# Kernel tuning notes

Hardware: AMD Instinct MI355X
Metric: run time of the kernel (lower is better)

## Reference

```python
import jax, jax.numpy as jnp
import numpy as np
import math

EMBED = 1024
HEADS = 16
DHEAD = 64
B, S = 2, 2048


def setup_inputs() -> dict:
    key = jax.random.key(0)
    k1, k2, k3, k4 = jax.random.split(key, 4)
    qs = jax.random.normal(k1, (B, S, EMBED), dtype=jnp.float32)
    # causal mask, broadcast over batch (mask==0 positions are masked out)
    mask = jnp.broadcast_to(jnp.tril(jnp.ones((S, S), dtype=jnp.int32)), (B, S, S))
    # torch Linear(embed, 3*H*D, bias=False): y = x @ W^T; store transposed [E, 3HD]
    Wqkv = jax.random.normal(k2, (EMBED, 3 * HEADS * DHEAD), dtype=jnp.float32) / math.sqrt(EMBED)
    Wout = jax.random.normal(k3, (HEADS * DHEAD, EMBED), dtype=jnp.float32) / math.sqrt(HEADS * DHEAD)
    bout = jax.random.normal(k4, (EMBED,), dtype=jnp.float32) * 0.01
    return {"qs": qs, "mask": mask, "Wqkv": Wqkv, "Wout": Wout, "bout": bout}


def reference(qs, mask, Wqkv, Wout, bout):
    b, s, _ = qs.shape
    # fused QKV projection -> (B, S, 3H, D), split into q/k/v chunks of H heads
    qkv = (qs @ Wqkv).reshape(b, s, 3 * HEADS, DHEAD)
    q, k, v = qkv[:, :, :HEADS], qkv[:, :, HEADS:2 * HEADS], qkv[:, :, 2 * HEADS:]
    # scores: (B, H, Sq, Sk)
    scores = jnp.einsum("bqhd,bkhd->bhqk", q, k) / math.sqrt(DHEAD)
    scores = jnp.where(mask[:, None, :, :] == 0, jnp.float32(-1e9), scores)
    attn = jax.nn.softmax(scores, axis=-1)
    out = jnp.einsum("bhqk,bkhd->bqhd", attn, v).reshape(b, s, HEADS * DHEAD)
    return out @ Wout + bout
```

## Files before the change

kernel.cpp:

```cpp
#include <hip/hip_runtime.h>
#include <hip/hip_bf16.h>
#include <stdint.h>


typedef __attribute__((ext_vector_type(8))) short  short8;
typedef __attribute__((ext_vector_type(4))) short  short4v;
typedef __attribute__((ext_vector_type(4))) float  float4v;

#define SOFTMAX_BIAS 17.3123405f
#define QSCALE 0.18033688f

__device__ __forceinline__ unsigned short f2bf(float f) {
  unsigned int u = __builtin_bit_cast(unsigned int, f);
  u += 0x7fffu + ((u >> 16) & 1u);
  return (unsigned short)(u >> 16);
}
__device__ __forceinline__ unsigned short f2bf_trunc(float f) {
  return (unsigned short)(__builtin_bit_cast(unsigned int, f) >> 16);
}
__device__ __forceinline__ float bf2f(unsigned short s) {
  unsigned int u = ((unsigned int)s) << 16;
  return __builtin_bit_cast(float, u);
}

__device__ __forceinline__ void async_copy16(const void* g, void* l) {
  __builtin_amdgcn_global_load_lds(
      (__attribute__((address_space(1))) unsigned int*)g,
      (__attribute__((address_space(3))) unsigned int*)l, 16, 0, 0);
}

__global__ void prep_kernel(const float* __restrict__ qs,
                            const float* __restrict__ Wqkv,
                            const float* __restrict__ Wout,
                            unsigned short* __restrict__ qs_bf,
                            unsigned short* __restrict__ WqkvT,
                            unsigned short* __restrict__ WoutT) {
  __shared__ float tbuf[32][33];
  const int blk = blockIdx.x, tid = threadIdx.x;
  if (blk < 4096) {
    int i = (blk * 256 + tid) * 4;
    float4v v = *(const float4v*)(qs + i);
    short4v o;
    o[0] = (short)f2bf(v[0]); o[1] = (short)f2bf(v[1]);
    o[2] = (short)f2bf(v[2]); o[3] = (short)f2bf(v[3]);
    *(short4v*)(qs_bf + i) = o;
  } else {
    const float* W; unsigned short* Wt; int N, t;
    if (blk < 4096 + 3072) { W = Wqkv; Wt = WqkvT; N = 3072; t = blk - 4096; }
    else                   { W = Wout; Wt = WoutT; N = 1024; t = blk - 7168; }
    const int tilesx = N >> 5;
    const int n0 = (t % tilesx) * 32, k0 = (t / tilesx) * 32;
    const int x = tid & 31, y = tid >> 5;
#pragma unroll
    for (int i = 0; i < 4; ++i)
      tbuf[y + i * 8][x] = W[(size_t)(k0 + y + i * 8) * N + n0 + x];
    __syncthreads();
#pragma unroll
    for (int i = 0; i < 4; ++i)
      Wt[(size_t)(n0 + y + i * 8) * 1024 + k0 + x] = f2bf(tbuf[x][y + i * 8]);
  }
}

__device__ __forceinline__ void gemm_bt_core(const unsigned short* __restrict__ A,
                                             const unsigned short* __restrict__ Bt,
                                             int m0, int n0,
                                             short* As, short* Bs,
                                             float4v (&acc)[4][4],
                                             int wm, int wn, int l15, int quad,
                                             int tid) {
  for (int k0 = 0; k0 < 1024; k0 += 32) {
    __syncthreads();
#pragma unroll
    for (int i = 0; i < 2; ++i) {
      int u = i * 256 + tid;
      int r = u >> 2, cpw = u & 3;
      int c = cpw ^ ((r >> 1) & 3);
      async_copy16(A  + (size_t)(m0 + r) * 1024 + k0 + c * 8, As + u * 8);
      async_copy16(Bt + (size_t)(n0 + r) * 1024 + k0 + c * 8, Bs + u * 8);
    }
    __syncthreads();

    short8 af[4], bfv[4];
#pragma unroll
    for (int t = 0; t < 4; ++t) {
      int ra = wm * 64 + t * 16 + l15;
      af[t]  = *(const short8*)(As + (ra * 4 + (quad ^ ((ra >> 1) & 3))) * 8);
      int rb = wn * 64 + t * 16 + l15;
      bfv[t] = *(const short8*)(Bs + (rb * 4 + (quad ^ ((rb >> 1) & 3))) * 8);
    }
#pragma unroll
    for (int mt = 0; mt < 4; ++mt)
#pragma unroll
      for (int nt = 0; nt < 4; ++nt)
        acc[mt][nt] = __builtin_amdgcn_mfma_f32_16x16x32_bf16(
            af[mt], bfv[nt], acc[mt][nt], 0, 0, 0);
  }
}

__global__ __launch_bounds__(256, 3)
void gemm_qkv_kernel(const unsigned short* __restrict__ Aq,
                     const unsigned short* __restrict__ Bt,
                     unsigned short* __restrict__ Qb,
                     unsigned short* __restrict__ Kb,
                     unsigned short* __restrict__ Vb) {
  __shared__ short As[128 * 32];
  __shared__ short Bs[128 * 32];
  const int tid = threadIdx.x, lane = tid & 63, w = tid >> 6;
  const int wm = w & 1, wn = w >> 1, l15 = lane & 15, quad = lane >> 4;
  const int m0 = blockIdx.x * 128, n0 = blockIdx.y * 128;

  float4v acc[4][4];
#pragma unroll
  for (int i = 0; i < 4; ++i)
#pragma unroll
    for (int j = 0; j < 4; ++j) acc[i][j] = (float4v)0.0f;

  gemm_bt_core(Aq, Bt, m0, n0, As, Bs, acc, wm, wn, l15, quad, tid);

#pragma unroll
  for (int nt = 0; nt < 4; ++nt) {
    int gn = n0 + wn * 64 + nt * 16 + l15;
    int j = gn >> 6, d = gn & 63;
    int g = j >> 4, h = j & 15;
    if (g == 2) {
#pragma unroll
      for (int mt = 0; mt < 4; ++mt) {
        int s0 = m0 + wm * 64 + mt * 16 + quad * 4;
        int b = s0 >> 11, s = s0 & 2047;
        short4v pk;
        pk[0] = (short)f2bf(acc[mt][nt][0]);
        pk[1] = (short)f2bf(acc[mt][nt][1]);
        pk[2] = (short)f2bf(acc[mt][nt][2]);
        pk[3] = (short)f2bf(acc[mt][nt][3]);
        *(short4v*)(Vb + (((size_t)(b * 16 + h) * 64 + d) << 11) + s) = pk;
      }
    } else {
#pragma unroll
      for (int mt = 0; mt < 4; ++mt) {
#pragma unroll
        for (int r = 0; r < 4; ++r) {
          int gm = m0 + wm * 64 + mt * 16 + quad * 4 + r;
          int b = gm >> 11, s = gm & 2047;
          float v = acc[mt][nt][r];
          if (g == 0)
            Qb[(((size_t)(b * 16 + h) * 2048 + s) << 6) + d] = f2bf(v * QSCALE);
          else
            Kb[(((size_t)(b * 16 + h) * 2048 + s) << 6) + d] = f2bf(v);
        }
      }
    }
  }
}

__global__ __launch_bounds__(256, 2)
void flash_attn_kernel(const unsigned short* __restrict__ Qb,
                       const unsigned short* __restrict__ Kb,
                       const unsigned short* __restrict__ Vb,
                       unsigned short* __restrict__ Pp0,
                       unsigned short* __restrict__ Pp1,
                       float* __restrict__ lws) {
  __shared__ unsigned short Kt[128 * 64];
  __shared__ unsigned short Vt[64 * 128];

  const int tid = threadIdx.x, lane = tid & 63, w = tid >> 6;
  const int l15 = lane & 15, quad = lane >> 4;
  const int rank = blockIdx.x >> 6;
  const int qt = 15 - rank;
  const int rem = blockIdx.x & 63;
  const int half = rem & 1;
  const int bh = rem >> 1;
  const int bb = bh >> 4, h = bh & 15;

  const int n = qt + 1, nh0 = (n + 1) >> 1;
  const int kt_lo = half ? nh0 : 0;
  const int kt_hi = half ? n : nh0;

  const unsigned short* Qg = Qb + (size_t)bh * 2048 * 64;
  const unsigned short* Kg = Kb + (size_t)bh * 2048 * 64;
  const unsigned short* Vg = Vb + (size_t)bh * 64 * 2048;
  unsigned short* Pw = Kt + w * (32 * 64);

  const int qb0 = qt * 128 + w * 32;

  short8 qf[2][2];
#pragma unroll
  for (int nt = 0; nt < 2; ++nt)
#pragma unroll
    for (int kc = 0; kc < 2; ++kc)
      qf[nt][kc] = *(const short8*)(Qg + (size_t)(qb0 + nt * 16 + l15) * 64 +
                                    kc * 32 + quad * 8);

  float l_s[2] = {0.0f, 0.0f};
  float4v o[4][2];
#pragma unroll
  for (int i = 0; i < 4; ++i) { o[i][0] = (float4v)0.0f; o[i][1] = (float4v)0.0f; }

  for (int kt = kt_lo; kt < kt_hi; ++kt) {
    const int kb = kt * 128;
    __syncthreads();
#pragma unroll
    for (int i = 0; i < 4; ++i) {
      int u = i * 256 + tid;
      int r = u >> 3, cp = u & 7;
      async_copy16(Kg + (size_t)(kb + r) * 64 + (cp ^ (r & 7)) * 8, Kt + u * 8);
    }
    __syncthreads();
#pragma unroll
    for (int i = 0; i < 4; ++i) {
      int u = i * 256 + tid;
      int r2 = u >> 4, cp2 = u & 15;
      async_copy16(Vg + (size_t)r2 * 2048 + kb + (cp2 ^ (r2 & 15)) * 8, Vt + u * 8);
    }

    float4v st[8][2];
    __builtin_amdgcn_s_setprio(1);
#pragma unroll
    for (int mt = 0; mt < 8; ++mt) {
      st[mt][0] = (float4v)(-SOFTMAX_BIAS);
      st[mt][1] = (float4v)(-SOFTMAX_BIAS);
      int key = mt * 16 + l15;
#pragma unroll
      for (int kc = 0; kc < 2; ++kc) {
        int cp = (kc * 4 + quad) ^ (key & 7);
        short8 a = *(const short8*)(Kt + key * 64 + cp * 8);
        st[mt][0] = __builtin_amdgcn_mfma_f32_16x16x32_bf16(a, qf[0][kc], st[mt][0], 0, 0, 0);
        st[mt][1] = __builtin_amdgcn_mfma_f32_16x16x32_bf16(a, qf[1][kc], st[mt][1], 0, 0, 0);
      }
    }
    __builtin_amdgcn_s_setprio(0);

    if (kt == qt) {
#pragma unroll
      for (int nt = 0; nt < 2; ++nt) {
        int qg = qb0 + nt * 16 + l15;
#pragma unroll
        for (int mt = 0; mt < 8; ++mt)
#pragma unroll
          for (int r = 0; r < 4; ++r) {
            int keyg = kb + mt * 16 + quad * 4 + r;
            if (keyg > qg) st[mt][nt][r] = -1e5f;
          }
      }
    }

#pragma unroll
    for (int nt = 0; nt < 2; ++nt) {
      float sum = 0.0f;
#pragma unroll
      for (int mt = 0; mt < 8; ++mt)
#pragma unroll
        for (int r = 0; r < 4; ++r) {
          float p = __builtin_amdgcn_exp2f(st[mt][nt][r]);
          st[mt][nt][r] = p;
          sum += p;
        }
      l_s[nt] += sum;
    }

    __syncthreads();

#pragma unroll
    for (int hf = 0; hf < 2; ++hf) {
#pragma unroll
      for (int nt = 0; nt < 2; ++nt) {
        int ql = nt * 16 + l15;
        unsigned short* prow = Pw + ql * 64;
#pragma unroll
        for (int mtl = 0; mtl < 4; ++mtl) {
          int mt = hf * 4 + mtl;
          short4v pk;
          pk[0] = (short)f2bf_trunc(st[mt][nt][0]);
          pk[1] = (short)f2bf_trunc(st[mt][nt][1]);
          pk[2] = (short)f2bf_trunc(st[mt][nt][2]);
          pk[3] = (short)f2bf_trunc(st[mt][nt][3]);
          int cp = (mtl * 2 + (quad >> 1)) ^ (l15 & 7);
          *(short4v*)(prow + cp * 8 + (quad & 1) * 4) = pk;
        }
      }
      __builtin_amdgcn_s_setprio(1);
#pragma unroll
      for (int kcl = 0; kcl < 2; ++kcl) {
        int kcg = hf * 2 + kcl;
        short8 pb[2];
#pragma unroll
        for (int nt = 0; nt < 2; ++nt) {
          int ql = nt * 16 + l15;
          int cp = (kcl * 4 + quad) ^ (l15 & 7);
          pb[nt] = *(const short8*)(Pw + ql * 64 + cp * 8);
        }
#pragma unroll
        for (int mtd = 0; mtd < 4; ++mtd) {
          int d = mtd * 16 + l15;
          int cp2 = (kcg * 4 + quad) ^ (d & 15);
          short8 a = *(const short8*)(Vt + d * 128 + cp2 * 8);
          o[mtd][0] = __builtin_amdgcn_mfma_f32_16x16x32_bf16(a, pb[0], o[mtd][0], 0, 0, 0);
          o[mtd][1] = __builtin_amdgcn_mfma_f32_16x16x32_bf16(a, pb[1], o[mtd][1], 0, 0, 0);
        }
      }
      __builtin_amdgcn_s_setprio(0);
    }
  }

  unsigned short* Pp = half ? Pp1 : Pp0;
#pragma unroll
  for (int nt = 0; nt < 2; ++nt) {
    float l = l_s[nt];
    l += __shfl_xor(l, 16);
    l += __shfl_xor(l, 32);
    int qg = qb0 + nt * 16 + l15;
    if (quad == 0) lws[half * 65536 + bh * 2048 + qg] = l;
#pragma unroll
    for (int mtd = 0; mtd < 4; ++mtd) {
      short4v pk;
      pk[0] = (short)f2bf(o[mtd][nt][0]);
      pk[1] = (short)f2bf(o[mtd][nt][1]);
      pk[2] = (short)f2bf(o[mtd][nt][2]);
      pk[3] = (short)f2bf(o[mtd][nt][3]);
      *(short4v*)(Pp + (size_t)(bb * 2048 + qg) * 1024 + h * 64 + mtd * 16 +
                  quad * 4) = pk;
    }
  }
}

__global__ void combine_kernel(const unsigned short* __restrict__ P0,
                               unsigned short* __restrict__ P1,
                               const float* __restrict__ lws) {
  int idx = (blockIdx.x * 256 + threadIdx.x) * 8;
  int t = idx >> 10, c = idx & 1023;
  int bh = (t >> 11) * 16 + (c >> 6);
  int q = t & 2047;
  float inv = 1.0f / (lws[bh * 2048 + q] + lws[65536 + bh * 2048 + q]);
  short8 a = *(const short8*)(P0 + idx);
  short8 b = *(const short8*)(P1 + idx);
  short8 r;
#pragma unroll
  for (int j = 0; j < 8; ++j)
    r[j] = (short)f2bf((bf2f((unsigned short)a[j]) +
                        bf2f((unsigned short)b[j])) * inv);
  *(short8*)(P1 + idx) = r;
}

__global__ __launch_bounds__(256, 3)
void gemm_out_kernel(const unsigned short* __restrict__ Aq,
                     const unsigned short* __restrict__ Bt,
                     const float* __restrict__ bout,
                     float* __restrict__ out) {
  __shared__ short As[64 * 32];
  __shared__ short Bs[128 * 32];
  const int tid = threadIdx.x, lane = tid & 63, w = tid >> 6;
  const int wm = w & 1, wn = w >> 1, l15 = lane & 15, quad = lane >> 4;
  const int m0 = blockIdx.x * 64, n0 = blockIdx.y * 128;

  float4v acc[2][4];
#pragma unroll
  for (int i = 0; i < 2; ++i)
#pragma unroll
    for (int j = 0; j < 4; ++j) acc[i][j] = (float4v)0.0f;

  for (int k0 = 0; k0 < 1024; k0 += 32) {
    __syncthreads();
    {
      int u = tid;
      int r = u >> 2, cpw = u & 3;
      int c = cpw ^ ((r >> 1) & 3);
      async_copy16(Aq + (size_t)(m0 + r) * 1024 + k0 + c * 8, As + u * 8);
    }
#pragma unroll
    for (int i = 0; i < 2; ++i) {
      int u = i * 256 + tid;
      int r = u >> 2, cpw = u & 3;
      int c = cpw ^ ((r >> 1) & 3);
      async_copy16(Bt + (size_t)(n0 + r) * 1024 + k0 + c * 8, Bs + u * 8);
    }
    __syncthreads();

    short8 af[2], bfv[4];
#pragma unroll
    for (int t = 0; t < 2; ++t) {
      int ra = wm * 32 + t * 16 + l15;
      af[t] = *(const short8*)(As + (ra * 4 + (quad ^ ((ra >> 1) & 3))) * 8);
    }
#pragma unroll
    for (int t = 0; t < 4; ++t) {
      int rb = wn * 64 + t * 16 + l15;
      bfv[t] = *(const short8*)(Bs + (rb * 4 + (quad ^ ((rb >> 1) & 3))) * 8);
    }
#pragma unroll
    for (int mt = 0; mt < 2; ++mt)
#pragma unroll
      for (int nt = 0; nt < 4; ++nt)
        acc[mt][nt] = __builtin_amdgcn_mfma_f32_16x16x32_bf16(
            af[mt], bfv[nt], acc[mt][nt], 0, 0, 0);
  }

#pragma unroll
  for (int nt = 0; nt < 4; ++nt) {
    int gn = n0 + wn * 64 + nt * 16 + l15;
    float bias = bout[gn];
#pragma unroll
    for (int mt = 0; mt < 2; ++mt) {
      int gmb = m0 + wm * 32 + mt * 16 + quad * 4;
#pragma unroll
      for (int r = 0; r < 4; ++r)
        out[(size_t)(gmb + r) * 1024 + gn] = acc[mt][nt][r] + bias;
    }
  }
}

extern "C" void kernel_launch(void* const* d_in, const int* in_sizes, int n_in,
                              void* d_out, int out_size, void* d_ws, size_t ws_size,
                              hipStream_t stream) {
  (void)in_sizes; (void)n_in; (void)out_size; (void)ws_size;
  const float* qs   = (const float*)d_in[0];
  const float* Wqkv = (const float*)d_in[2];
  const float* Wout = (const float*)d_in[3];
  const float* bout = (const float*)d_in[4];
  float* out = (float*)d_out;

  unsigned short* qs_bf = (unsigned short*)d_ws;
  unsigned short* WqkvT = qs_bf + 4096 * 1024;
  unsigned short* WoutT = WqkvT + 3072 * 1024;
  unsigned short* Qb    = WoutT + 1024 * 1024;
  unsigned short* Kb    = Qb + 32 * 2048 * 64;
  unsigned short* Vb    = Kb + 32 * 2048 * 64;
  unsigned short* Ob    = Vb + 32 * 2048 * 64;

  unsigned short* P0 = qs_bf;
  float*          lw = (float*)WqkvT;
  unsigned short* P1 = Ob;

  prep_kernel<<<8192, 256, 0, stream>>>(qs, Wqkv, Wout, qs_bf, WqkvT, WoutT);
  gemm_qkv_kernel<<<dim3(32, 24), 256, 0, stream>>>(qs_bf, WqkvT, Qb, Kb, Vb);
  flash_attn_kernel<<<1024, 256, 0, stream>>>(Qb, Kb, Vb, P0, P1, lw);
  combine_kernel<<<2048, 256, 0, stream>>>(P0, P1, lw);
  gemm_out_kernel<<<dim3(64, 8), 256, 0, stream>>>(P1, WoutT, bout, out);
}
```

Before: 189.7 us.

## Rewrite QKV GEMM with 256x256 tiles, double-buffered async LDS pipeline

Replaces the 128x128, K=32 QKV projection GEMM with a 512-thread 256x256-tile kernel using K=64 stages, double-buffered in a 128KB LDS buffer. Global-to-LDS async copies for the next tile are interleaved with MFMA groups under explicit barriers, vmcnt waits and setprio. A block-id swizzle improves L2 locality. It aims to hide load latency and raise arithmetic intensity per LDS byte, but gives only 192 blocks (fewer than 256 CUs), which may leave CUs idle.

```diff
diff --git a/kernel.cpp b/kernel.cpp
--- a/kernel.cpp
+++ b/kernel.cpp
@@ -61,87 +61,150 @@
   }
 }
 
-__device__ __forceinline__ void gemm_bt_core(const unsigned short* __restrict__ A,
-                                             const unsigned short* __restrict__ Bt,
-                                             int m0, int n0,
-                                             short* As, short* Bs,
-                                             float4v (&acc)[4][4],
-                                             int wm, int wn, int l15, int quad,
-                                             int tid) {
-  for (int k0 = 0; k0 < 1024; k0 += 32) {
-    __syncthreads();
-#pragma unroll
-    for (int i = 0; i < 2; ++i) {
-      int u = i * 256 + tid;
-      int r = u >> 2, cpw = u & 3;
-      int c = cpw ^ ((r >> 1) & 3);
-      async_copy16(A  + (size_t)(m0 + r) * 1024 + k0 + c * 8, As + u * 8);
-      async_copy16(Bt + (size_t)(n0 + r) * 1024 + k0 + c * 8, Bs + u * 8);
-    }
-    __syncthreads();
-
-    short8 af[4], bfv[4];
-#pragma unroll
-    for (int t = 0; t < 4; ++t) {
-      int ra = wm * 64 + t * 16 + l15;
-      af[t]  = *(const short8*)(As + (ra * 4 + (quad ^ ((ra >> 1) & 3))) * 8);
-      int rb = wn * 64 + t * 16 + l15;
-      bfv[t] = *(const short8*)(Bs + (rb * 4 + (quad ^ ((rb >> 1) & 3))) * 8);
-    }
-#pragma unroll
-    for (int mt = 0; mt < 4; ++mt)
-#pragma unroll
-      for (int nt = 0; nt < 4; ++nt)
-        acc[mt][nt] = __builtin_amdgcn_mfma_f32_16x16x32_bf16(
-            af[mt], bfv[nt], acc[mt][nt], 0, 0, 0);
-  }
-}
-
-__global__ __launch_bounds__(256, 3)
+#define STAGE_HALF(G, grow0, ktile, dstbase)                               \
+  {                                                                        \
+    _Pragma("unroll")                                                      \
+    for (int rnd_ = 0; rnd_ < 2; ++rnd_) {                                 \
+      int e_ = rnd_ * 512 + tid;                                           \
+      int r_ = e_ >> 3, cp_ = e_ & 7;                                      \
+      async_copy16(G + (size_t)((grow0) + r_) * 1024 + (ktile) * 64 +      \
+                       ((cp_ ^ (r_ & 7)) * 8),                             \
+                   (dstbase) + e_ * 8);                                    \
+    }                                                                      \
+  }
+#define STAGE_A(t, h) STAGE_HALF(Aq, m0 + (h) * 128, (t),                  \
+                                 ldsb + ((t) & 1) * 32768 + (h) * 8192)
+#define STAGE_B(t, h) STAGE_HALF(Bt, n0 + (h) * 128, (t),                  \
+                                 ldsb + ((t) & 1) * 32768 + 16384 + (h) * 8192)
+#define LOADB(Bx)                                                          \
+  {                                                                        \
+    _Pragma("unroll") for (int nf_ = 0; nf_ < 4; ++nf_) {                  \
+      rb[nf_][0] = *(const short8*)((Bx) + (rb0 + nf_ * 16) * 64 + scol0); \
+      rb[nf_][1] = *(const short8*)((Bx) + (rb0 + nf_ * 16) * 64 + scol1); \
+    }                                                                      \
+  }
+#define LOADA(Ax, mfb)                                                     \
+  {                                                                        \
+    _Pragma("unroll") for (int d_ = 0; d_ < 2; ++d_) {                     \
+      ra[d_][0] = *(const short8*)((Ax) + (ra0 + ((mfb) + d_) * 16) * 64 + scol0); \
+      ra[d_][1] = *(const short8*)((Ax) + (ra0 + ((mfb) + d_) * 16) * 64 + scol1); \
+    }                                                                      \
+  }
+#define MFMA16(q)                                                          \
+  {                                                                        \
+    __builtin_amdgcn_s_setprio(1);                                         \
+    _Pragma("unroll") for (int kc_ = 0; kc_ < 2; ++kc_)                    \
+    _Pragma("unroll") for (int d_ = 0; d_ < 2; ++d_)                       \
+    _Pragma("unroll") for (int nf_ = 0; nf_ < 4; ++nf_)                    \
+      acc[(q) * 2 + d_][nf_] = __builtin_amdgcn_mfma_f32_16x16x32_bf16(    \
+          ra[d_][kc_], rb[nf_][kc_], acc[(q) * 2 + d_][nf_], 0, 0, 0);     \
+    __builtin_amdgcn_s_setprio(0);                                         \
+  }
+#define BAR_                                                               \
+  __builtin_amdgcn_sched_barrier(0);                                       \
+  __builtin_amdgcn_s_barrier();                                            \
+  __builtin_amdgcn_sched_barrier(0)
+
+__global__ __launch_bounds__(512, 2)
 void gemm_qkv_kernel(const unsigned short* __restrict__ Aq,
                      const unsigned short* __restrict__ Bt,
                      unsigned short* __restrict__ Qb,
                      unsigned short* __restrict__ Kb,
                      unsigned short* __restrict__ Vb) {
-  __shared__ short As[128 * 32];
-  __shared__ short Bs[128 * 32];
+  __shared__ unsigned short ldsb[65536];
   const int tid = threadIdx.x, lane = tid & 63, w = tid >> 6;
-  const int wm = w & 1, wn = w >> 1, l15 = lane & 15, quad = lane >> 4;
-  const int m0 = blockIdx.x * 128, n0 = blockIdx.y * 128;
-
-  float4v acc[4][4];
-#pragma unroll
-  for (int i = 0; i < 4; ++i)
+  const int wm = w >> 2, wn = w & 3;
+  const int l15 = lane & 15, quad = lane >> 4;
+
+  const int bid = blockIdx.x;
+  const int swz = (bid & 7) * 24 + (bid >> 3);
+  const int m0 = (swz / 12) * 256, n0 = (swz % 12) * 256;
+
+  const int scol0 = (quad * 8) ^ ((l15 & 7) << 3);
+  const int scol1 = (32 + quad * 8) ^ ((l15 & 7) << 3);
+  const unsigned short* A0 = ldsb + wm * 8192;
+  const unsigned short* B0 = ldsb + 16384 + (wn >> 1) * 8192;
+  const unsigned short* A1 = A0 + 32768;
+  const unsigned short* B1 = B0 + 32768;
+  const int ra0 = l15;
+  const int rb0 = (wn & 1) * 64 + l15;
+
+  float4v acc[8][4];
+#pragma unroll
+  for (int i = 0; i < 8; ++i)
 #pragma unroll
     for (int j = 0; j < 4; ++j) acc[i][j] = (float4v)0.0f;
-
-  gemm_bt_core(Aq, Bt, m0, n0, As, Bs, acc, wm, wn, l15, quad, tid);
-
-#pragma unroll
-  for (int nt = 0; nt < 4; ++nt) {
-    int gn = n0 + wn * 64 + nt * 16 + l15;
-    int j = gn >> 6, d = gn & 63;
-    int g = j >> 4, h = j & 15;
-    if (g == 2) {
-#pragma unroll
-      for (int mt = 0; mt < 4; ++mt) {
-        int s0 = m0 + wm * 64 + mt * 16 + quad * 4;
-        int b = s0 >> 11, s = s0 & 2047;
+  short8 ra[2][2], rb[4][2];
+
+  STAGE_A(0, 0); STAGE_A(0, 1); STAGE_B(0, 0); STAGE_B(0, 1);
+  STAGE_B(1, 0); STAGE_B(1, 1);
+  asm volatile("s_waitcnt vmcnt(4)" ::: "memory");
+  BAR_;
+
+  for (int i = 0; i < 8; ++i) {
+    const int t1  = 2 * i + 1;
+    const int tc0 = (2 * i + 2 <= 14) ? 2 * i + 2 : 14;
+    const int tc1 = (2 * i + 3 <= 15) ? 2 * i + 3 : 15;
+    LOADB(B0); LOADA(A0, 0);
+    STAGE_A(t1, 0); STAGE_A(t1, 1);
+    BAR_; MFMA16(0); BAR_;
+    LOADA(A0, 2);
+    STAGE_B(tc0, 0);
+    BAR_; MFMA16(1); BAR_;
+    LOADA(A0, 4);
+    STAGE_B(tc0, 1);
+    BAR_; MFMA16(2); BAR_;
+    LOADA(A0, 6);
+    BAR_; MFMA16(3);
+    asm volatile("s_waitcnt vmcnt(4)" ::: "memory");
+    BAR_;
+    LOADB(B1); LOADA(A1, 0);
+    STAGE_A(tc0, 0);
+    BAR_; MFMA16(0); BAR_;
+    LOADA(A1, 2);
+    STAGE_A(tc0, 1);
+    BAR_; MFMA16(1); BAR_;
+    LOADA(A1, 4);
+    STAGE_B(tc1, 0);
+    BAR_; MFMA16(2); BAR_;
+    LOADA(A1, 6);
+    STAGE_B(tc1, 1);
+    BAR_; MFMA16(3);
+    asm volatile("s_waitcnt vmcnt(4)" ::: "memory");
+    BAR_;
+  }
+
+  const int gnbase = n0 + wn * 64;
+  const int j = gnbase >> 6;
+  const int g = j >> 4, h = j & 15;
+  if (g == 2) {
+#pragma unroll
+    for (int mf = 0; mf < 8; ++mf) {
+      int gm0 = m0 + wm * 128 + mf * 16 + quad * 4;
+      int b = gm0 >> 11, s = gm0 & 2047;
+#pragma unroll
+      for (int nf = 0; nf < 4; ++nf) {
+        int d = nf * 16 + l15;
         short4v pk;
-        pk[0] = (short)f2bf(acc[mt][nt][0]);
-        pk[1] = (short)f2bf(acc[mt][nt][1]);
-        pk[2] = (short)f2bf(acc[mt][nt][2]);
-        pk[3] = (short)f2bf(acc[mt][nt][3]);
+        pk[0] = (short)f2bf(acc[mf][nf][0]);
+        pk[1] = (short)f2bf(acc[mf][nf][1]);
+        pk[2] = (short)f2bf(acc[mf][nf][2]);
+        pk[3] = (short)f2bf(acc[mf][nf][3]);
         *(short4v*)(Vb + (((size_t)(b * 16 + h) * 64 + d) << 11) + s) = pk;
       }
-    } else {
-#pragma unroll
-      for (int mt = 0; mt < 4; ++mt) {
+    }
+  } else {
+#pragma unroll
+    for (int mf = 0; mf < 8; ++mf) {
+      int gm0 = m0 + wm * 128 + mf * 16 + quad * 4;
+#pragma unroll
+      for (int nf = 0; nf < 4; ++nf) {
+        int d = nf * 16 + l15;
 #pragma unroll
         for (int r = 0; r < 4; ++r) {
-          int gm = m0 + wm * 64 + mt * 16 + quad * 4 + r;
+          int gm = gm0 + r;
           int b = gm >> 11, s = gm & 2047;
-          float v = acc[mt][nt][r];
+          float v = acc[mf][nf][r];
           if (g == 0)
             Qb[(((size_t)(b * 16 + h) * 2048 + s) << 6) + d] = f2bf(v * QSCALE);
           else
@@ -382,8 +445,8 @@
     }
 #pragma unroll
     for (int t = 0; t < 4; ++t) {
-      int rb = wn * 64 + t * 16 + l15;
-      bfv[t] = *(const short8*)(Bs + (rb * 4 + (quad ^ ((rb >> 1) & 3))) * 8);
+      int rbx = wn * 64 + t * 16 + l15;
+      bfv[t] = *(const short8*)(Bs + (rbx * 4 + (quad ^ ((rbx >> 1) & 3))) * 8);
     }
 #pragma unroll
     for (int mt = 0; mt < 2; ++mt)
@@ -430,7 +493,7 @@
   unsigned short* P1 = Ob;
 
   prep_kernel<<<8192, 256, 0, stream>>>(qs, Wqkv, Wout, qs_bf, WqkvT, WoutT);
-  gemm_qkv_kernel<<<dim3(32, 24), 256, 0, stream>>>(qs_bf, WqkvT, Qb, Kb, Vb);
+  gemm_qkv_kernel<<<192, 512, 0, stream>>>(qs_bf, WqkvT, Qb, Kb, Vb);
   flash_attn_kernel<<<1024, 256, 0, stream>>>(Qb, Kb, Vb, P0, P1, lw);
   combine_kernel<<<2048, 256, 0, stream>>>(P0, P1, lw);
   gemm_out_kernel<<<dim3(64, 8), 256, 0, stream>>>(P1, WoutT, bout, out);
```

Measured after the change: 193.8 us. 2.1% more time.

## Fuse split-KV combine into output projection GEMM A-tile load

Applied to the files above, without the earlier changes.

Removes the separate combine kernel. The output GEMM now reads both partial attention outputs and the two softmax denominators directly, then normalizes and sums them while staging the A tile into shared memory. Next-iteration A data is register-prefetched to hide load latency. This saves one launch and one round trip of the combined activation through memory. In exchange, the combine arithmetic is repeated across the 8 N-column blocks, and A is now loaded synchronously instead of by async copy.

```diff
diff --git a/kernel.cpp b/kernel.cpp
--- a/kernel.cpp
+++ b/kernel.cpp
@@ -322,26 +322,10 @@
   }
 }
 
-__global__ void combine_kernel(const unsigned short* __restrict__ P0,
-                               unsigned short* __restrict__ P1,
-                               const float* __restrict__ lws) {
-  int idx = (blockIdx.x * 256 + threadIdx.x) * 8;
-  int t = idx >> 10, c = idx & 1023;
-  int bh = (t >> 11) * 16 + (c >> 6);
-  int q = t & 2047;
-  float inv = 1.0f / (lws[bh * 2048 + q] + lws[65536 + bh * 2048 + q]);
-  short8 a = *(const short8*)(P0 + idx);
-  short8 b = *(const short8*)(P1 + idx);
-  short8 r;
-#pragma unroll
-  for (int j = 0; j < 8; ++j)
-    r[j] = (short)f2bf((bf2f((unsigned short)a[j]) +
-                        bf2f((unsigned short)b[j])) * inv);
-  *(short8*)(P1 + idx) = r;
-}
-
 __global__ __launch_bounds__(256, 3)
-void gemm_out_kernel(const unsigned short* __restrict__ Aq,
+void gemm_out_kernel(const unsigned short* __restrict__ P0,
+                     const unsigned short* __restrict__ P1,
+                     const float* __restrict__ lws,
                      const unsigned short* __restrict__ Bt,
                      const float* __restrict__ bout,
                      float* __restrict__ out) {
@@ -351,20 +335,26 @@
   const int wm = w & 1, wn = w >> 1, l15 = lane & 15, quad = lane >> 4;
   const int m0 = blockIdx.x * 64, n0 = blockIdx.y * 128;
 
+  const int rA = tid >> 2, cpwA = tid & 3;
+  const int cA = cpwA ^ ((rA >> 1) & 3);
+  const int mA = m0 + rA;
+  const int bA = mA >> 11, sA = mA & 2047;
+  const size_t arow = (size_t)mA * 1024;
+  const float* lw0 = lws + (size_t)bA * 16 * 2048 + sA;
+  const float* lw1 = lw0 + 65536;
+
   float4v acc[2][4];
 #pragma unroll
   for (int i = 0; i < 2; ++i)
 #pragma unroll
     for (int j = 0; j < 4; ++j) acc[i][j] = (float4v)0.0f;
 
+  short8 a0n = *(const short8*)(P0 + arow + cA * 8);
+  short8 a1n = *(const short8*)(P1 + arow + cA * 8);
+  float ln = lw0[0] + lw1[0];
+
   for (int k0 = 0; k0 < 1024; k0 += 32) {
     __syncthreads();
-    {
-      int u = tid;
-      int r = u >> 2, cpw = u & 3;
-      int c = cpw ^ ((r >> 1) & 3);
-      async_copy16(Aq + (size_t)(m0 + r) * 1024 + k0 + c * 8, As + u * 8);
-    }
 #pragma unroll
     for (int i = 0; i < 2; ++i) {
       int u = i * 256 + tid;
@@ -372,6 +362,21 @@
       int c = cpw ^ ((r >> 1) & 3);
       async_copy16(Bt + (size_t)(n0 + r) * 1024 + k0 + c * 8, Bs + u * 8);
     }
+    short8 a0c = a0n, a1c = a1n;
+    float lc = ln;
+    if (k0 + 32 < 1024) {
+      a0n = *(const short8*)(P0 + arow + (k0 + 32) + cA * 8);
+      a1n = *(const short8*)(P1 + arow + (k0 + 32) + cA * 8);
+      int hn = (k0 + 32) >> 6;
+      ln = lw0[hn * 2048] + lw1[hn * 2048];
+    }
+    float inv = 1.0f / lc;
+    short8 cmb;
+#pragma unroll
+    for (int j = 0; j < 8; ++j)
+      cmb[j] = (short)f2bf((bf2f((unsigned short)a0c[j]) +
+                            bf2f((unsigned short)a1c[j])) * inv);
+    *(short8*)(As + tid * 8) = cmb;
     __syncthreads();
 
     short8 af[2], bfv[4];
@@ -382,8 +387,8 @@
     }
 #pragma unroll
     for (int t = 0; t < 4; ++t) {
-      int rb = wn * 64 + t * 16 + l15;
-      bfv[t] = *(const short8*)(Bs + (rb * 4 + (quad ^ ((rb >> 1) & 3))) * 8);
+      int rbx = wn * 64 + t * 16 + l15;
+      bfv[t] = *(const short8*)(Bs + (rbx * 4 + (quad ^ ((rbx >> 1) & 3))) * 8);
     }
 #pragma unroll
     for (int mt = 0; mt < 2; ++mt)
@@ -432,6 +437,5 @@
   prep_kernel<<<8192, 256, 0, stream>>>(qs, Wqkv, Wout, qs_bf, WqkvT, WoutT);
   gemm_qkv_kernel<<<dim3(32, 24), 256, 0, stream>>>(qs_bf, WqkvT, Qb, Kb, Vb);
   flash_attn_kernel<<<1024, 256, 0, stream>>>(Qb, Kb, Vb, P0, P1, lw);
-  combine_kernel<<<2048, 256, 0, stream>>>(P0, P1, lw);
-  gemm_out_kernel<<<dim3(64, 8), 256, 0, stream>>>(P1, WoutT, bout, out);
-}
+  gemm_out_kernel<<<dim3(64, 8), 256, 0, stream>>>(P0, P1, lw, WoutT, bout, out);
+}
```

Result: slower. 194.0 us (+2.2%).
